# Optimization experiments

Measured on AMD Instinct MI355X. Metric: run time of the kernel, lower is better.

Reference implementation:

```python
import jax, jax.numpy as jnp
import numpy as np

D = 2048      # hidden_size
H = 16        # heads
HD = D // H   # head_dim = 128
FF = 8192     # intermediate_size
B = 4
S = 2048
FACTOR = 0.5  # mod_router_factor
EPS = 1e-6


def setup_inputs() -> dict:
    key = jax.random.key(0)
    ks = jax.random.split(key, 10)
    w = lambda k, shape: jax.random.normal(k, shape, jnp.float32) * 0.02
    return {
        "hidden_states": jax.random.normal(ks[0], (B, S, D), jnp.float32),
        "position_ids": jnp.arange(S, dtype=jnp.int32)[None, :],
        "mod_target_mask": jnp.ones((B, S), dtype=bool),
        "attention_mask_2d": jnp.ones((B, S), dtype=bool),
        "router_w": w(ks[1], (D,)),
        "ln1_w": jnp.ones((D,), jnp.float32),
        "ln2_w": jnp.ones((D,), jnp.float32),
        "Wq": w(ks[2], (D, D)),
        "Wk": w(ks[3], (D, D)),
        "Wv": w(ks[4], (D, D)),
        "Wo": w(ks[5], (D, D)),
        "W1": w(ks[6], (D, FF)),
        "W2": w(ks[7], (FF, D)),
    }


def _rmsnorm(x, w):
    return x * jax.lax.rsqrt(jnp.mean(x * x, axis=-1, keepdims=True) + EPS) * w


def _rope(x, pos):
    # x: [B,K,H,HD], pos: [B,K]
    half = HD // 2
    freqs = 1.0 / (10000.0 ** (jnp.arange(half, dtype=jnp.float32) / half))
    ang = pos[:, :, None].astype(jnp.float32) * freqs  # [B,K,half]
    cos = jnp.cos(ang)[:, :, None, :]
    sin = jnp.sin(ang)[:, :, None, :]
    x1, x2 = x[..., :half], x[..., half:]
    return jnp.concatenate([x1 * cos - x2 * sin, x2 * cos + x1 * sin], axis=-1)


def reference(hidden_states, position_ids, mod_target_mask, attention_mask_2d,
              router_w, ln1_w, ln2_w, Wq, Wk, Wv, Wo, W1, W2):
    Bq, Sq, _ = hidden_states.shape
    K = int(Sq * FACTOR)  # static top-k length (all rows fully mod-targeted)

    # --- token router ---
    logits = jnp.einsum('bsd,d->bs', hidden_states, router_w)
    logits = jnp.where(mod_target_mask, logits, -jnp.inf)
    weights = jax.nn.sigmoid(logits)  # weight_normalization: sigmoid * 1.0 + 0.0

    # --- top-k dispatch (indices sorted to preserve sequence order, matching
    # torch boolean-mask gather of kept tokens) ---
    _, idx = jax.lax.top_k(weights, K)
    idx = jnp.sort(idx, axis=1)                       # [B,K]
    bidx = jnp.arange(Bq)[:, None]
    kept = hidden_states[bidx, idx]                   # [B,K,D] residual
    pos = jnp.broadcast_to(position_ids, (Bq, Sq))[bidx, idx]

    # --- decoder layer (Llama-style pre-norm block) on kept tokens ---
    h1 = _rmsnorm(kept, ln1_w)
    q = _rope((h1 @ Wq).reshape(Bq, K, H, HD), pos)
    k = _rope((h1 @ Wk).reshape(Bq, K, H, HD), pos)
    v = (h1 @ Wv).reshape(Bq, K, H, HD)
    scores = jnp.einsum('bqhd,bkhd->bhqk', q, k) / np.sqrt(HD).astype(np.float32)
    causal = jnp.tril(jnp.ones((K, K), dtype=bool))
    scores = jnp.where(causal, scores, jnp.finfo(scores.dtype).min)
    attn = jax.nn.softmax(scores, axis=-1)
    ao = jnp.einsum('bhqk,bkhd->bqhd', attn, v).reshape(Bq, K, D) @ Wo
    h2 = kept + ao
    mlp = jax.nn.gelu(_rmsnorm(h2, ln2_w) @ W1) @ W2
    delta = ao + mlp  # forward_return_residual: layer_out - residual

    # --- combine: hidden[kept]=delta; hidden[target]*=w; hidden[kept]+=residual ---
    out = hidden_states.at[bidx, idx].set(delta)
    out = jnp.where(mod_target_mask[..., None], out * weights[..., None], out)
    out = out.at[bidx, idx].add(kept)
    return out
```

## Files before the change

### kernel.cpp

```cpp
#include <hip/hip_runtime.h>
#include <stdint.h>

#define Dm 2048
#define Hn 16
#define HDm 128
#define FFm 8192
#define Bm 4
#define Sm 2048
#define Km 1024

typedef __attribute__((ext_vector_type(4))) float f32x4;
typedef __attribute__((ext_vector_type(8))) short s16x8;
typedef unsigned short u16;
typedef unsigned int u32;

__device__ __forceinline__ float bf_lo(u32 u){ u32 x = u << 16; return __builtin_bit_cast(float, x); }
__device__ __forceinline__ float bf_hi(u32 u){ u32 x = u & 0xffff0000u; return __builtin_bit_cast(float, x); }
__device__ __forceinline__ float bfu(u16 u){ u32 x = ((u32)u) << 16; return __builtin_bit_cast(float, x); }
__device__ __forceinline__ u16 f2bf(float f){
  u32 u = __builtin_bit_cast(u32, f);
  u += 0x7fffu + ((u >> 16) & 1u);
  return (u16)(u >> 16);
}
__device__ __forceinline__ u32 pack2(float a, float b){
  return (u32)f2bf(a) | ((u32)f2bf(b) << 16);
}
__device__ __forceinline__ void unpack8(uint4 a, float* f){
  f[0]=bf_lo(a.x); f[1]=bf_hi(a.x); f[2]=bf_lo(a.y); f[3]=bf_hi(a.y);
  f[4]=bf_lo(a.z); f[5]=bf_hi(a.z); f[6]=bf_lo(a.w); f[7]=bf_hi(a.w);
}
__device__ __forceinline__ uint4 pack8(const float* f){
  uint4 o; o.x=pack2(f[0],f[1]); o.y=pack2(f[2],f[3]); o.z=pack2(f[4],f[5]); o.w=pack2(f[6],f[7]); return o;
}
__device__ __forceinline__ void load8_in(const void* p, size_t off, int fp32, float* f){
  if (fp32){
    const float* pf = (const float*)p + off;
    float4 a = *(const float4*)pf;
    float4 b = *(const float4*)(pf + 4);
    f[0]=a.x; f[1]=a.y; f[2]=a.z; f[3]=a.w;
    f[4]=b.x; f[5]=b.y; f[6]=b.z; f[7]=b.w;
  } else {
    uint4 a = *(const uint4*)((const u16*)p + off);
    unpack8(a, f);
  }
}
__device__ __forceinline__ float gelu_f(float x){
  float t = tanhf(0.7978845608028654f*(x + 0.044715f*x*x*x));
  return 0.5f*x*(1.0f + t);
}
__device__ __forceinline__ float block_sum256(float s){
  #pragma unroll
  for (int off = 32; off; off >>= 1) s += __shfl_xor(s, off);
  __shared__ float red[4];
  int lane = threadIdx.x & 63, w = threadIdx.x >> 6;
  if (lane == 0) red[w] = s;
  __syncthreads();
  return red[0] + red[1] + red[2] + red[3];
}
__device__ __forceinline__ void gload_lds16(const u16* g, u16* l){
  __builtin_amdgcn_global_load_lds((const __attribute__((address_space(1))) void*)g,
                                   (__attribute__((address_space(3))) void*)l, 16, 0, 0);
}

__global__ __launch_bounds__(256) void sniff_kernel(const u32* __restrict__ hs, int* __restrict__ flag){
  __shared__ int s;
  if (threadIdx.x == 0) s = 0;
  __syncthreads();
  int bad = 0;
  for (int i = threadIdx.x; i < 4096; i += 256){
    u32 w = hs[i];
    float lo = bf_lo(w), hi = bf_hi(w);
    if (!(fabsf(lo) < 1000.f && fabsf(hi) < 1000.f)) bad = 1;
  }
  if (bad) atomicOr(&s, 1);
  __syncthreads();
  if (threadIdx.x == 0) flag[0] = s;
}

__global__ __launch_bounds__(256) void router_kernel(const void* __restrict__ hs, const void* __restrict__ rw,
                                                     const int* __restrict__ dflag,
                                                     float* __restrict__ weights, int* __restrict__ selmap){
  int fp32 = *dflag;
  int row = blockIdx.x, t = threadIdx.x;
  float a[8], b8[8];
  load8_in(hs, (size_t)row*Dm + t*8, fp32, a);
  load8_in(rw, (size_t)t*8, fp32, b8);
  float s = 0.f;
  #pragma unroll
  for (int i = 0; i < 8; i++) s += a[i]*b8[i];
  float tot = block_sum256(s);
  if (t == 0){
    weights[row] = 1.0f/(1.0f + expf(-tot));
    selmap[row] = -1;
  }
}

__global__ __launch_bounds__(1024) void topk_kernel(const float* __restrict__ weights, const int* __restrict__ position_ids,
                                                    int* __restrict__ idx, int* __restrict__ pos, int* __restrict__ selmap){
  int b = blockIdx.x, t = threadIdx.x;
  __shared__ float v[Sm];
  __shared__ int id[Sm];
  v[t] = weights[b*Sm + t];             id[t] = t;
  v[t+1024] = weights[b*Sm + t + 1024]; id[t+1024] = t + 1024;
  for (int size = 2; size <= Sm; size <<= 1){
    for (int stride = size >> 1; stride > 0; stride >>= 1){
      __syncthreads();
      int lo = ((t & ~(stride-1)) << 1) | (t & (stride-1));
      int hi = lo + stride;
      bool up = (lo & size) == 0;
      float va = v[lo], vb = v[hi]; int ia = id[lo], ib = id[hi];
      bool aFirst = (va > vb) || (va == vb && ia < ib);
      if (up ? !aFirst : aFirst){ v[lo]=vb; v[hi]=va; id[lo]=ib; id[hi]=ia; }
    }
  }
  __syncthreads();
  for (int size = 2; size <= Km; size <<= 1){
    for (int stride = size >> 1; stride > 0; stride >>= 1){
      __syncthreads();
      if (t < Km/2){
        int lo = ((t & ~(stride-1)) << 1) | (t & (stride-1));
        int hi = lo + stride;
        bool up = (lo & size) == 0;
        int ia = id[lo], ib = id[hi];
        bool aFirst = ia < ib;
        if (up ? !aFirst : aFirst){ id[lo]=ib; id[hi]=ia; }
      }
    }
  }
  __syncthreads();
  if (t < Km){
    int iv = id[t];
    idx[b*Km + t] = iv;
    pos[b*Km + t] = position_ids[iv];
    selmap[b*Sm + iv] = t;
  }
}

__global__ __launch_bounds__(256) void gather_rmsnorm(const void* __restrict__ hs, const int* __restrict__ idx,
                                                      const void* __restrict__ ln1, const int* __restrict__ dflag,
                                                      u16* __restrict__ h1){
  int fp32 = *dflag;
  int g = blockIdx.x, t = threadIdx.x;
  int b = g >> 10;
  int row = idx[g];
  float f[8];
  load8_in(hs, ((size_t)b*Sm + row)*Dm + t*8, fp32, f);
  float ss = 0.f;
  #pragma unroll
  for (int i = 0; i < 8; i++) ss += f[i]*f[i];
  float tot = block_sum256(ss);
  float scale = rsqrtf(tot * (1.0f/Dm) + 1e-6f);
  float lw[8];
  load8_in(ln1, (size_t)t*8, fp32, lw);
  float o[8];
  #pragma unroll
  for (int i = 0; i < 8; i++) o[i] = f[i]*scale*lw[i];
  ((uint4*)(h1 + (size_t)g*Dm))[t] = pack8(o);
}

__global__ __launch_bounds__(256) void h2norm_kernel(const void* __restrict__ hs, const int* __restrict__ idx,
                                                     const u16* __restrict__ ao, const void* __restrict__ ln2,
                                                     const int* __restrict__ dflag, u16* __restrict__ h2n){
  int fp32 = *dflag;
  int g = blockIdx.x, t = threadIdx.x;
  int b = g >> 10;
  int row = idx[g];
  float ke[8], av[8];
  load8_in(hs, ((size_t)b*Sm + row)*Dm + t*8, fp32, ke);
  unpack8(((const uint4*)(ao + (size_t)g*Dm))[t], av);
  float f[8]; float ss = 0.f;
  #pragma unroll
  for (int i = 0; i < 8; i++){ f[i] = ke[i] + av[i]; ss += f[i]*f[i]; }
  float tot = block_sum256(ss);
  float scale = rsqrtf(tot * (1.0f/Dm) + 1e-6f);
  float lw[8];
  load8_in(ln2, (size_t)t*8, fp32, lw);
  float o[8];
  #pragma unroll
  for (int i = 0; i < 8; i++) o[i] = f[i]*scale*lw[i];
  ((uint4*)(h2n + (size_t)g*Dm))[t] = pack8(o);
}

__global__ __launch_bounds__(256) void transpose_k(const void* __restrict__ src, const int* __restrict__ dflag,
                                                   u16* __restrict__ dst, int R, int C, int ldS, size_t srcOff){
  int fp32 = *dflag;
  __shared__ u16 tile[64][72];
  int c0 = blockIdx.x << 6, r0 = blockIdx.y << 6;
  int t = threadIdx.x;
  int rr = t >> 3, cc = (t & 7) * 8;
  #pragma unroll
  for (int p = 0; p < 2; p++){
    float f[8];
    load8_in(src, srcOff + (size_t)(r0 + rr + p*32) * ldS + c0 + cc, fp32, f);
    u16 tmp[8];
    #pragma unroll
    for (int j = 0; j < 8; j++) tmp[j] = f2bf(f[j]);
    *(uint4*)&tile[rr + p*32][cc] = *(const uint4*)tmp;
  }
  __syncthreads();
  int col = t >> 3, r8 = (t & 7) * 8;
  #pragma unroll
  for (int p = 0; p < 2; p++){
    u16 tmp[8];
    #pragma unroll
    for (int j = 0; j < 8; j++) tmp[j] = tile[r8 + j][col + p*32];
    *(uint4*)(dst + (size_t)(c0 + col + p*32) * R + r0 + r8) = *(const uint4*)tmp;
  }
}

__global__ __launch_bounds__(256) void transpose_qkv(const void* __restrict__ Wq, const void* __restrict__ Wk,
                                                     const void* __restrict__ Wv, const int* __restrict__ dflag,
                                                     u16* __restrict__ dqk, u16* __restrict__ dv){
  int fp32 = *dflag;
  __shared__ u16 tile[64][72];
  int z = blockIdx.z;
  const void* src = (z == 0) ? Wq : (z == 1) ? Wk : Wv;
  u16* dst = (z == 0) ? dqk : (z == 1) ? dqk + (size_t)2048*2048 : dv;
  int c0 = blockIdx.x << 6, r0 = blockIdx.y << 6;
  int t = threadIdx.x;
  int rr = t >> 3, cc = (t & 7) * 8;
  #pragma unroll
  for (int p = 0; p < 2; p++){
    float f[8];
    load8_in(src, (size_t)(r0 + rr + p*32) * 2048 + c0 + cc, fp32, f);
    u16 tmp[8];
    #pragma unroll
    for (int j = 0; j < 8; j++) tmp[j] = f2bf(f[j]);
    *(uint4*)&tile[rr + p*32][cc] = *(const uint4*)tmp;
  }
  __syncthreads();
  int col = t >> 3, r8 = (t & 7) * 8;
  #pragma unroll
  for (int p = 0; p < 2; p++){
    u16 tmp[8];
    #pragma unroll
    for (int j = 0; j < 8; j++) tmp[j] = tile[r8 + j][col + p*32];
    *(uint4*)(dst + (size_t)(c0 + col + p*32) * 2048 + r0 + r8) = *(const uint4*)tmp;
  }
}

__global__ __launch_bounds__(256) void transpose_v(const u16* __restrict__ src, u16* __restrict__ dst){
  __shared__ u16 tile[64][72];
  int bh = blockIdx.z; int b = bh >> 4, h = bh & 15;
  int key0 = blockIdx.x << 6;
  int d0 = blockIdx.y << 6;
  int t = threadIdx.x;
  int rr = t >> 3, cc = (t & 7) * 8;
  #pragma unroll
  for (int p = 0; p < 2; p++){
    uint4 a = *(const uint4*)(src + ((size_t)(b*Km + key0 + rr + p*32))*Dm + h*HDm + d0 + cc);
    *(uint4*)&tile[rr + p*32][cc] = a;
  }
  __syncthreads();
  int col = t >> 3, r8 = (t & 7) * 8;
  #pragma unroll
  for (int p = 0; p < 2; p++){
    u16 tmp[8];
    #pragma unroll
    for (int j = 0; j < 8; j++) tmp[j] = tile[r8 + j][col + p*32];
    *(uint4*)(dst + ((size_t)bh*HDm + d0 + col + p*32)*Km + key0 + r8) = *(const uint4*)tmp;
  }
}

template<int BN>
__global__ __launch_bounds__(512, 2) void gemm256(const u16* __restrict__ A, const u16* __restrict__ BT,
                                                  u16* __restrict__ Cmat, int Kd, int lda, int ldb, int ldc,
                                                  int do_gelu, int accum){
  extern __shared__ u16 lds[];
  constexpr int WC    = BN / 4;
  constexpr int NREP  = BN / 64;
  constexpr int BTILE = BN * 64;
  constexpr int BROWS = BN / 8;
  constexpr int NSTGB = BN / 64;
  const int t    = threadIdx.x;
  const int lane = t & 63, wid = t >> 6;
  const int wr = wid >> 2, wc = wid & 3;
  const int l16 = lane & 15, quad = lane >> 4;
  const int bid0 = (int)(blockIdx.y * gridDim.x + blockIdx.x);
  const int cpx  = (int)(gridDim.x * gridDim.y) >> 3;
  const int swz  = (bid0 & 7) * cpx + (bid0 >> 3);
  const int m0 = (swz % (int)gridDim.x) * 256;
  const int n0 = (swz / (int)gridDim.x) * BN;

  const int lrow = lane >> 3;
  const int csw  = (lane & 7) ^ lrow;
  const u16* gA = A  + (size_t)(m0 + wid*32    + lrow) * lda + csw*8;
  const u16* gB = BT + (size_t)(n0 + wid*BROWS + lrow) * ldb + csw*8;

  f32x4 acc[8][NREP];
  #pragma unroll
  for (int i = 0; i < 8; i++)
    #pragma unroll
    for (int j = 0; j < NREP; j++) acc[i][j] = (f32x4){0.f,0.f,0.f,0.f};

  auto STAGE = [&](int buf, int kt){
    u16* la = lds + buf*16384 + (wid*32)*64;
    #pragma unroll
    for (int s = 0; s < 4; s++)
      gload_lds16(gA + (size_t)(s*8)*lda + kt*64, la + (s*8)*64);
    u16* lb = lds + 32768 + buf*BTILE + (wid*BROWS)*64;
    #pragma unroll
    for (int s = 0; s < NSTGB; s++)
      gload_lds16(gB + (size_t)(s*8)*ldb + kt*64, lb + (s*8)*64);
  };

  const int NT = Kd >> 6;
  STAGE(0, 0);
  for (int kt = 0; kt < NT; kt++){
    const int cur = kt & 1;
    if (kt + 1 < NT){
      STAGE(cur ^ 1, kt + 1);
      if constexpr (BN == 256) asm volatile("s_waitcnt vmcnt(8)" ::: "memory");
      else                     asm volatile("s_waitcnt vmcnt(6)" ::: "memory");
    } else {
      asm volatile("s_waitcnt vmcnt(0)" ::: "memory");
    }
    __builtin_amdgcn_s_barrier();
    __builtin_amdgcn_sched_barrier(0);
    const u16* LA = lds + cur*16384;
    const u16* LB = lds + 32768 + cur*BTILE;
    const int rsw = l16 & 7;
    s16x8 bf[NREP][2];
    #pragma unroll
    for (int ni = 0; ni < NREP; ni++)
      #pragma unroll
      for (int ks = 0; ks < 2; ks++)
        bf[ni][ks] = *(const s16x8*)(LB + (wc*WC + ni*16 + l16)*64 + ((ks*4 + quad) ^ rsw)*8);
    #pragma unroll
    for (int mi = 0; mi < 8; mi++){
      const u16* ar = LA + (wr*128 + mi*16 + l16)*64;
      s16x8 a0 = *(const s16x8*)(ar + ((quad     ^ rsw)*8));
      s16x8 a1 = *(const s16x8*)(ar + (((4+quad) ^ rsw)*8));
      __builtin_amdgcn_s_setprio(1);
      #pragma unroll
      for (int ni = 0; ni < NREP; ni++){
        acc[mi][ni] = __builtin_amdgcn_mfma_f32_16x16x32_bf16(a0, bf[ni][0], acc[mi][ni], 0, 0, 0);
        acc[mi][ni] = __builtin_amdgcn_mfma_f32_16x16x32_bf16(a1, bf[ni][1], acc[mi][ni], 0, 0, 0);
      }
      __builtin_amdgcn_s_setprio(0);
    }
    asm volatile("" ::: "memory");
    __builtin_amdgcn_s_barrier();
    __builtin_amdgcn_sched_barrier(0);
  }

  if (accum){
    __syncthreads();
    float* Cf = (float*)lds;
    #pragma unroll
    for (int mi = 0; mi < 8; mi++)
      #pragma unroll
      for (int ni = 0; ni < NREP; ni++){
        int rb = wr*128 + mi*16 + quad*4;
        int col = wc*WC + ni*16 + l16;
        #pragma unroll
        for (int r = 0; r < 4; r++) Cf[(rb + r)*BN + col] = acc[mi][ni][r];
      }
    __syncthreads();
    constexpr int CH = (256*BN)/4096;
    #pragma unroll
    for (int i = 0; i < CH; i++){
      int off = i*4096 + t*8;
      int row = off / BN, col = off % BN;
      u16* cp = Cmat + (size_t)(m0 + row)*ldc + n0 + col;
      uint4 old = *(const uint4*)cp;
      float f[8]; unpack8(old, f);
      float4 a = *(const float4*)(Cf + off);
      float4 b2 = *(const float4*)(Cf + off + 4);
      float o[8] = {a.x+f[0], a.y+f[1], a.z+f[2], a.w+f[3],
                    b2.x+f[4], b2.y+f[5], b2.z+f[6], b2.w+f[7]};
      *(uint4*)cp = pack8(o);
    }
  } else {
    __syncthreads();
    u16* Ct = lds;
    #pragma unroll
    for (int mi = 0; mi < 8; mi++)
      #pragma unroll
      for (int ni = 0; ni < NREP; ni++){
        int rb = wr*128 + mi*16 + quad*4;
        int col = wc*WC + ni*16 + l16;
        #pragma unroll
        for (int r = 0; r < 4; r++){
          float v = acc[mi][ni][r];
          if (do_gelu) v = gelu_f(v);
          Ct[(rb + r)*BN + col] = f2bf(v);
        }
      }
    __syncthreads();
    constexpr int CH = (256*BN)/4096;
    #pragma unroll
    for (int i = 0; i < CH; i++){
      int off = i*4096 + t*8;
      int row = off / BN, col = off % BN;
      uint4 v = *(const uint4*)(Ct + off);
      *(uint4*)(Cmat + (size_t)(m0 + row)*ldc + n0 + col) = v;
    }
  }
}

__global__ __launch_bounds__(256) void rope_kernel(u16* __restrict__ qkb, const int* __restrict__ pos){
  int tid = blockIdx.x*256 + threadIdx.x;
  int row = tid >> 6, d = tid & 63;
  int grow = row >> 4, h = row & 15;
  float p = (float)pos[grow];
  float freq = exp2f(-0.20762050593589063f * (float)d);
  float ang = p * freq;
  float cs = cosf(ang), sn = sinf(ang);
  size_t base = (size_t)grow * 4096 + h*HDm + d;
  float x1 = bfu(qkb[base]), x2 = bfu(qkb[base+64]);
  qkb[base]    = f2bf(x1*cs - x2*sn);
  qkb[base+64] = f2bf(x2*cs + x1*sn);
  x1 = bfu(qkb[base+2048]); x2 = bfu(qkb[base+2048+64]);
  qkb[base+2048]    = f2bf(x1*cs - x2*sn);
  qkb[base+2048+64] = f2bf(x2*cs + x1*sn);
}

__global__ __launch_bounds__(256, 2) void attn_mfma(const u16* __restrict__ qk, const u16* __restrict__ vt,
                                                    u16* __restrict__ o){
  __shared__ __align__(16) u16 Plds[4][32][72];
  const int w = threadIdx.x >> 6;
  const int lane = threadIdx.x & 63;
  const int l16 = lane & 15, quad = lane >> 4;
  const int bh = blockIdx.y;
  const int b = bh >> 4, h = bh & 15;
  const int bxr = (int)gridDim.x - 1 - (int)blockIdx.x;
  const int q0 = bxr * 128 + w * 32;
  const int QLD = 4096;

  s16x8 aq[2][4];
  #pragma unroll
  for (int qt = 0; qt < 2; qt++){
    const u16* qrow = qk + ((size_t)b*Km + q0 + qt*16 + l16)*QLD + h*HDm;
    #pragma unroll
    for (int kk = 0; kk < 4; kk++) aq[qt][kk] = *(const s16x8*)(qrow + kk*32 + quad*8);
  }
  const u16* kbase = qk + (size_t)b*Km*QLD + 2048 + h*HDm;
  const u16* vth   = vt + (size_t)bh * HDm * Km;

  f32x4 accO[2][8];
  #pragma unroll
  for (int qt = 0; qt < 2; qt++)
    #pragma unroll
    for (int n = 0; n < 8; n++) accO[qt][n] = (f32x4){0.f,0.f,0.f,0.f};
  float mrow[2][4], lrow[2][4];
  #pragma unroll
  for (int qt = 0; qt < 2; qt++)
    #pragma unroll
    for (int r = 0; r < 4; r++){ mrow[qt][r] = -1e30f; lrow[qt][r] = 0.f; }

  const float c = 0.08838834764831845f * 1.4426950408889634f;
  const int qmax = q0 + 31;

  s16x8 bk[4][4];
  #pragma unroll
  for (int half = 0; half < 4; half++){
    const u16* krow = kbase + (size_t)(half*16 + l16)*QLD;
    #pragma unroll
    for (int kk = 0; kk < 4; kk++) bk[half][kk] = *(const s16x8*)(krow + kk*32 + quad*8);
  }

  for (int kt = 0; kt <= qmax; kt += 64){
    float sv[4][2][4];
    #pragma unroll
    for (int half = 0; half < 4; half++){
      int key = kt + half*16 + l16;
      #pragma unroll
      for (int qt = 0; qt < 2; qt++){
        f32x4 s = (f32x4){0.f,0.f,0.f,0.f};
        #pragma unroll
        for (int kk = 0; kk < 4; kk++)
          s = __builtin_amdgcn_mfma_f32_16x16x32_bf16(aq[qt][kk], bk[half][kk], s, 0, 0, 0);
        #pragma unroll
        for (int r = 0; r < 4; r++)
          sv[half][qt][r] = (key <= q0 + qt*16 + quad*4 + r) ? s[r]*c : -1e30f;
      }
    }
    if (kt + 64 <= qmax){
      #pragma unroll
      for (int half = 0; half < 4; half++){
        const u16* krow = kbase + (size_t)(kt + 64 + half*16 + l16)*QLD;
        #pragma unroll
        for (int kk = 0; kk < 4; kk++) bk[half][kk] = *(const s16x8*)(krow + kk*32 + quad*8);
      }
    }
    float alpha[2][4];
    #pragma unroll
    for (int qt = 0; qt < 2; qt++){
      #pragma unroll
      for (int r = 0; r < 4; r++){
        float cm = fmaxf(fmaxf(sv[0][qt][r], sv[1][qt][r]), fmaxf(sv[2][qt][r], sv[3][qt][r]));
        cm = fmaxf(cm, __shfl_xor(cm, 1));
        cm = fmaxf(cm, __shfl_xor(cm, 2));
        cm = fmaxf(cm, __shfl_xor(cm, 4));
        cm = fmaxf(cm, __shfl_xor(cm, 8));
        float mn = fmaxf(mrow[qt][r], cm);
        alpha[qt][r] = __builtin_amdgcn_exp2f(mrow[qt][r] - mn);
        mrow[qt][r] = mn;
        float ps = 0.f;
        #pragma unroll
        for (int hh = 0; hh < 4; hh++){
          float p = __builtin_amdgcn_exp2f(sv[hh][qt][r] - mn);
          u16 u = f2bf(p);
          Plds[w][qt*16 + quad*4 + r][hh*16 + l16] = u;
          ps += bfu(u);
        }
        ps += __shfl_xor(ps, 1);
        ps += __shfl_xor(ps, 2);
        ps += __shfl_xor(ps, 4);
        ps += __shfl_xor(ps, 8);
        lrow[qt][r] = lrow[qt][r]*alpha[qt][r] + ps;
      }
    }
    asm volatile("s_waitcnt lgkmcnt(0)" ::: "memory");
    __builtin_amdgcn_sched_barrier(0);
    s16x8 ap[2][2];
    #pragma unroll
    for (int qt = 0; qt < 2; qt++){
      ap[qt][0] = *(const s16x8*)&Plds[w][qt*16 + l16][quad*8];
      ap[qt][1] = *(const s16x8*)&Plds[w][qt*16 + l16][32 + quad*8];
    }
    #pragma unroll
    for (int qt = 0; qt < 2; qt++)
      #pragma unroll
      for (int n = 0; n < 8; n++)
        #pragma unroll
        for (int r = 0; r < 4; r++) accO[qt][n][r] *= alpha[qt][r];
    #pragma unroll
    for (int n = 0; n < 8; n++){
      const u16* vrow = vth + (size_t)(n*16 + l16)*Km + kt;
      s16x8 bv0 = *(const s16x8*)(vrow + quad*8);
      s16x8 bv1 = *(const s16x8*)(vrow + 32 + quad*8);
      accO[0][n] = __builtin_amdgcn_mfma_f32_16x16x32_bf16(ap[0][0], bv0, accO[0][n], 0, 0, 0);
      accO[0][n] = __builtin_amdgcn_mfma_f32_16x16x32_bf16(ap[0][1], bv1, accO[0][n], 0, 0, 0);
      accO[1][n] = __builtin_amdgcn_mfma_f32_16x16x32_bf16(ap[1][0], bv0, accO[1][n], 0, 0, 0);
      accO[1][n] = __builtin_amdgcn_mfma_f32_16x16x32_bf16(ap[1][1], bv1, accO[1][n], 0, 0, 0);
    }
  }

  #pragma unroll
  for (int qt = 0; qt < 2; qt++){
    float inv[4];
    #pragma unroll
    for (int r = 0; r < 4; r++) inv[r] = 1.0f / lrow[qt][r];
    #pragma unroll
    for (int n = 0; n < 8; n++)
      #pragma unroll
      for (int r = 0; r < 4; r++){
        size_t off = ((size_t)b*Km + q0 + qt*16 + quad*4 + r)*Dm + h*HDm + n*16 + l16;
        o[off] = f2bf(accO[qt][n][r]*inv[r]);
      }
  }
}

__global__ __launch_bounds__(256) void final_kernel(const void* __restrict__ hidden, const float* __restrict__ weights,
                                                    const int* __restrict__ selmap, const u16* __restrict__ delta,
                                                    const int* __restrict__ dflag, void* __restrict__ outv){
  int fp32 = *dflag;
  int row = blockIdx.x, t = threadIdx.x;
  int b = row >> 11;
  float w = weights[row];
  int sel = selmap[row];
  float hv[8];
  load8_in(hidden, (size_t)row*Dm + t*8, fp32, hv);
  float f[8];
  if (sel >= 0){
    size_t ko = ((size_t)(b*Km + sel))*Dm;
    float dv[8];
    unpack8(((const uint4*)(delta+ko))[t], dv);
    #pragma unroll
    for (int i = 0; i < 8; i++) f[i] = dv[i]*w + hv[i];
  } else {
    #pragma unroll
    for (int i = 0; i < 8; i++) f[i] = hv[i]*w;
  }
  if (fp32){
    float* o = (float*)outv + (size_t)row*Dm + t*8;
    float4 x; x.x=f[0]; x.y=f[1]; x.z=f[2]; x.w=f[3];
    float4 y; y.x=f[4]; y.y=f[5]; y.z=f[6]; y.w=f[7];
    *(float4*)o = x; *(float4*)(o+4) = y;
  } else {
    ((uint4*)((u16*)outv + (size_t)row*Dm))[t] = pack8(f);
  }
}

extern "C" void kernel_launch(void* const* d_in, const int* in_sizes, int n_in,
                              void* d_out, int out_size, void* d_ws, size_t ws_size,
                              hipStream_t stream){
  (void)in_sizes; (void)n_in; (void)out_size; (void)ws_size;
  const void* hidden      = d_in[0];
  const int* position_ids = (const int*)d_in[1];
  const void* router_w = d_in[4];
  const void* ln1 = d_in[5];
  const void* ln2 = d_in[6];
  const void* Wq  = d_in[7];
  const void* Wk  = d_in[8];
  const void* Wv  = d_in[9];
  const void* Wo  = d_in[10];
  const void* W1  = d_in[11];
  const void* W2  = d_in[12];
  char* ws = (char*)d_ws;
  const size_t MB = 1ull << 20;
  float* weights = (float*)ws;
  int* idx     = (int*)(ws + 32768);
  int* pos     = (int*)(ws + 49152);
  int* selmap  = (int*)(ws + 65536);
  int* dflag   = (int*)(ws + 98304);
  u16* bufB  = (u16*)(ws +  1*MB);
  u16* qkbuf = (u16*)(ws + 17*MB);
  u16* aoB   = qkbuf;
  u16* TWbig = (u16*)(ws + 33*MB);
  u16* TW8   = (u16*)(ws + 49*MB);
  u16* vb   = (u16*)d_out;
  u16* TWqk = (u16*)d_out + 8ull*MB;
  u16* VT   = TWqk;
  u16* gbuf = (u16*)d_out;

  sniff_kernel<<<1, 256, 0, stream>>>((const u32*)hidden, dflag);
  router_kernel<<<Bm*Sm, 256, 0, stream>>>(hidden, router_w, dflag, weights, selmap);
  topk_kernel<<<Bm, 1024, 0, stream>>>(weights, position_ids, idx, pos, selmap);
  gather_rmsnorm<<<Bm*Km, 256, 0, stream>>>(hidden, idx, ln1, dflag, bufB);

  transpose_qkv<<<dim3(32,32,3), 256, 0, stream>>>(Wq, Wk, Wv, dflag, TWqk, TW8);
  gemm256<256><<<dim3(16,16), 512, 131072, stream>>>(bufB, TWqk, qkbuf, Dm, Dm, Dm, 4096, 0, 0);
  gemm256<128><<<dim3(16,16), 512, 98304, stream>>>(bufB, TW8, vb, Dm, Dm, Dm, Dm, 0, 0);

  rope_kernel<<<16384, 256, 0, stream>>>(qkbuf, pos);
  transpose_v<<<dim3(16,2,64), 256, 0, stream>>>(vb, VT);
  attn_mfma<<<dim3(8,64), 256, 0, stream>>>(qkbuf, VT, bufB);

  transpose_k<<<dim3(32,32), 256, 0, stream>>>(Wo, dflag, TW8, Dm, Dm, Dm, 0);
  gemm256<128><<<dim3(16,16), 512, 98304, stream>>>(bufB, TW8, aoB, Dm, Dm, Dm, Dm, 0, 0);

  h2norm_kernel<<<Bm*Km, 256, 0, stream>>>(hidden, idx, aoB, ln2, dflag, bufB);

  for (int c = 0; c < 2; c++){
    transpose_k<<<dim3(64,32), 256, 0, stream>>>(W1, dflag, TWbig, Dm, 4096, FFm, (size_t)c*4096);
    gemm256<256><<<dim3(16,16), 512, 131072, stream>>>(bufB, TWbig, gbuf, Dm, Dm, Dm, 4096, 1, 0);
    transpose_k<<<dim3(32,64), 256, 0, stream>>>(W2, dflag, TWbig, 4096, Dm, Dm, (size_t)c*4096*Dm);
    gemm256<128><<<dim3(16,16), 512, 131072, stream>>>(gbuf, TWbig, aoB, 4096, 4096, 4096, Dm, 0, 1);
  }

  final_kernel<<<Bm*Sm, 256, 0, stream>>>(hidden, weights, selmap, aoB, dflag, d_out);
}
```

Measured before the change: 967.6 us.

## Stage attention K/V tiles into double-buffered LDS shared across waves

The attention kernel now loads K and V chunks cooperatively into swizzled, double-buffered LDS with async global-to-LDS loads, with block barriers between stages. Before, each wave read K and V straight from global memory. The change is meant to cut redundant global traffic across the four waves and to overlap the next chunk's load with the current chunk's compute. It also raises MFMA priority with setprio around the matrix ops. In exchange it needs about 82KB of dynamic LDS, which reduces occupancy, and every wave must iterate to the block's maximum key chunk, doing extra fully masked work.

```diff
diff --git a/kernel.cpp b/kernel.cpp
--- a/kernel.cpp
+++ b/kernel.cpp
@@ -416,9 +416,15 @@
   qkb[base+2048+64] = f2bf(x2*cs + x1*sn);
 }
 
-__global__ __launch_bounds__(256, 2) void attn_mfma(const u16* __restrict__ qk, const u16* __restrict__ vt,
-                                                    u16* __restrict__ o){
-  __shared__ __align__(16) u16 Plds[4][32][72];
+__global__ __launch_bounds__(256) void attn_mfma(const u16* __restrict__ qk, const u16* __restrict__ vt,
+                                                 u16* __restrict__ o){
+  extern __shared__ __align__(16) u16 alds[];
+  typedef u16 KTile[64][128];
+  typedef u16 VTile[128][64];
+  typedef u16 PTile[32][72];
+  KTile* Kl = (KTile*)alds;
+  VTile* Vl = (VTile*)(alds + 16384);
+  PTile* Pl = (PTile*)(alds + 32768);
   const int w = threadIdx.x >> 6;
   const int lane = threadIdx.x & 63;
   const int l16 = lane & 15, quad = lane >> 4;
@@ -426,6 +432,7 @@
   const int b = bh >> 4, h = bh & 15;
   const int bxr = (int)gridDim.x - 1 - (int)blockIdx.x;
   const int q0 = bxr * 128 + w * 32;
+  const int nch = 2 * (bxr + 1);
   const int QLD = 4096;
 
   s16x8 aq[2][4];
@@ -438,6 +445,23 @@
   const u16* kbase = qk + (size_t)b*Km*QLD + 2048 + h*HDm;
   const u16* vth   = vt + (size_t)bh * HDm * Km;
 
+  auto STAGE = [&](int buf, int c){
+    #pragma unroll
+    for (int j = 0; j < 4; j++){
+      int row  = w*16 + j*4 + (lane >> 4);
+      int slot = lane & 15;
+      gload_lds16(kbase + (size_t)(c*64 + row)*QLD + ((slot ^ (row & 7))*8),
+                  &Kl[buf][w*16 + j*4][0]);
+    }
+    #pragma unroll
+    for (int j = 0; j < 4; j++){
+      int row  = w*32 + j*8 + (lane >> 3);
+      int slot = lane & 7;
+      gload_lds16(vth + (size_t)row*Km + c*64 + ((slot ^ (row & 7))*8),
+                  &Vl[buf][w*32 + j*8][0]);
+    }
+  };
+
   f32x4 accO[2][8];
   #pragma unroll
   for (int qt = 0; qt < 2; qt++)
@@ -450,39 +474,41 @@
     for (int r = 0; r < 4; r++){ mrow[qt][r] = -1e30f; lrow[qt][r] = 0.f; }
 
   const float c = 0.08838834764831845f * 1.4426950408889634f;
-  const int qmax = q0 + 31;
-
-  s16x8 bk[4][4];
-  #pragma unroll
-  for (int half = 0; half < 4; half++){
-    const u16* krow = kbase + (size_t)(half*16 + l16)*QLD;
-    #pragma unroll
-    for (int kk = 0; kk < 4; kk++) bk[half][kk] = *(const s16x8*)(krow + kk*32 + quad*8);
-  }
-
-  for (int kt = 0; kt <= qmax; kt += 64){
+
+  STAGE(0, 0);
+  for (int t = 0; t < nch; t++){
+    const int cur = t & 1;
+    if (t + 1 < nch){
+      STAGE(cur ^ 1, t + 1);
+      asm volatile("s_waitcnt vmcnt(8)" ::: "memory");
+    } else {
+      asm volatile("s_waitcnt vmcnt(0)" ::: "memory");
+    }
+    __builtin_amdgcn_s_barrier();
+    __builtin_amdgcn_sched_barrier(0);
+    const int kt = t * 64;
     float sv[4][2][4];
     #pragma unroll
     for (int half = 0; half < 4; half++){
+      const int krow = half*16 + l16;
+      const int rx = krow & 7;
+      s16x8 bk[4];
+      #pragma unroll
+      for (int kk = 0; kk < 4; kk++)
+        bk[kk] = *(const s16x8*)&Kl[cur][krow][((kk*4 + quad) ^ rx)*8];
       int key = kt + half*16 + l16;
+      __builtin_amdgcn_s_setprio(1);
       #pragma unroll
       for (int qt = 0; qt < 2; qt++){
         f32x4 s = (f32x4){0.f,0.f,0.f,0.f};
         #pragma unroll
         for (int kk = 0; kk < 4; kk++)
-          s = __builtin_amdgcn_mfma_f32_16x16x32_bf16(aq[qt][kk], bk[half][kk], s, 0, 0, 0);
+          s = __builtin_amdgcn_mfma_f32_16x16x32_bf16(aq[qt][kk], bk[kk], s, 0, 0, 0);
         #pragma unroll
         for (int r = 0; r < 4; r++)
           sv[half][qt][r] = (key <= q0 + qt*16 + quad*4 + r) ? s[r]*c : -1e30f;
       }
-    }
-    if (kt + 64 <= qmax){
-      #pragma unroll
-      for (int half = 0; half < 4; half++){
-        const u16* krow = kbase + (size_t)(kt + 64 + half*16 + l16)*QLD;
-        #pragma unroll
-        for (int kk = 0; kk < 4; kk++) bk[half][kk] = *(const s16x8*)(krow + kk*32 + quad*8);
-      }
+      __builtin_amdgcn_s_setprio(0);
     }
     float alpha[2][4];
     #pragma unroll
@@ -502,7 +528,7 @@
         for (int hh = 0; hh < 4; hh++){
           float p = __builtin_amdgcn_exp2f(sv[hh][qt][r] - mn);
           u16 u = f2bf(p);
-          Plds[w][qt*16 + quad*4 + r][hh*16 + l16] = u;
+          Pl[w][qt*16 + quad*4 + r][hh*16 + l16] = u;
           ps += bfu(u);
         }
         ps += __shfl_xor(ps, 1);
@@ -517,8 +543,8 @@
     s16x8 ap[2][2];
     #pragma unroll
     for (int qt = 0; qt < 2; qt++){
-      ap[qt][0] = *(const s16x8*)&Plds[w][qt*16 + l16][quad*8];
-      ap[qt][1] = *(const s16x8*)&Plds[w][qt*16 + l16][32 + quad*8];
+      ap[qt][0] = *(const s16x8*)&Pl[w][qt*16 + l16][quad*8];
+      ap[qt][1] = *(const s16x8*)&Pl[w][qt*16 + l16][32 + quad*8];
     }
     #pragma unroll
     for (int qt = 0; qt < 2; qt++)
@@ -528,14 +554,20 @@
         for (int r = 0; r < 4; r++) accO[qt][n][r] *= alpha[qt][r];
     #pragma unroll
     for (int n = 0; n < 8; n++){
-      const u16* vrow = vth + (size_t)(n*16 + l16)*Km + kt;
-      s16x8 bv0 = *(const s16x8*)(vrow + quad*8);
-      s16x8 bv1 = *(const s16x8*)(vrow + 32 + quad*8);
+      const int vrow = n*16 + l16;
+      const int rx = vrow & 7;
+      s16x8 bv0 = *(const s16x8*)&Vl[cur][vrow][((quad)     ^ rx)*8];
+      s16x8 bv1 = *(const s16x8*)&Vl[cur][vrow][((4 + quad) ^ rx)*8];
+      __builtin_amdgcn_s_setprio(1);
       accO[0][n] = __builtin_amdgcn_mfma_f32_16x16x32_bf16(ap[0][0], bv0, accO[0][n], 0, 0, 0);
       accO[0][n] = __builtin_amdgcn_mfma_f32_16x16x32_bf16(ap[0][1], bv1, accO[0][n], 0, 0, 0);
       accO[1][n] = __builtin_amdgcn_mfma_f32_16x16x32_bf16(ap[1][0], bv0, accO[1][n], 0, 0, 0);
       accO[1][n] = __builtin_amdgcn_mfma_f32_16x16x32_bf16(ap[1][1], bv1, accO[1][n], 0, 0, 0);
-    }
+      __builtin_amdgcn_s_setprio(0);
+    }
+    asm volatile("" ::: "memory");
+    __builtin_amdgcn_s_barrier();
+    __builtin_amdgcn_sched_barrier(0);
   }
 
   #pragma unroll
@@ -627,7 +659,7 @@
 
   rope_kernel<<<16384, 256, 0, stream>>>(qkbuf, pos);
   transpose_v<<<dim3(16,2,64), 256, 0, stream>>>(vb, VT);
-  attn_mfma<<<dim3(8,64), 256, 0, stream>>>(qkbuf, VT, bufB);
+  attn_mfma<<<dim3(8,64), 256, 83968, stream>>>(qkbuf, VT, bufB);
 
   transpose_k<<<dim3(32,32), 256, 0, stream>>>(Wo, dflag, TW8, Dm, Dm, Dm, 0);
   gemm256<128><<<dim3(16,16), 512, 98304, stream>>>(bufB, TW8, aoB, Dm, Dm, Dm, Dm, 0, 0);
```

Result: no change. 954.1 us (-1.4%).
